# Optimization experiments

Hardware: AMD Instinct MI355X
Metric: run time of the kernel (lower is better)

The kernel has to match this reference:

```python
import jax, jax.numpy as jnp
import numpy as np

DMODEL = 1024
N_EXPERTS = 8
EXPERT_SIZE = 4096
TOPK = 2
B, S = 2, 2048


def setup_inputs() -> dict:
    key = jax.random.key(0)
    ks = jax.random.split(key, 6)
    std = EXPERT_SIZE ** (-0.5)  # init_expert_weights: normal(0, expert_size**-0.5 * weight_scale)
    x = jax.random.normal(ks[0], (B, S, DMODEL), dtype=jnp.float32)
    gate_w = 0.02 * jax.random.normal(ks[1], (N_EXPERTS, DMODEL), dtype=jnp.float32)
    w1 = std * jax.random.normal(ks[2], (N_EXPERTS, EXPERT_SIZE, DMODEL), dtype=jnp.float32)
    b1 = jnp.zeros((N_EXPERTS, EXPERT_SIZE), dtype=jnp.float32)
    w2 = std * jax.random.normal(ks[3], (N_EXPERTS, DMODEL, EXPERT_SIZE), dtype=jnp.float32)
    b2 = jnp.zeros((N_EXPERTS, DMODEL), dtype=jnp.float32)
    return {"x": x, "gate_w": gate_w, "w1": w1, "b1": b1, "w2": w2, "b2": b2}


def reference(x, gate_w, w1, b1, w2, b2):
    # Router: gate linear (no bias) -> softmax -> top-k expert selection
    logits = jnp.einsum('bsd,ed->bse', x, gate_w)          # [B,S,E]
    probs = jax.nn.softmax(logits, axis=-1)                # gate_softmax
    top_w, top_i = jax.lax.top_k(probs, TOPK)              # [B,S,K]
    # Scatter top-k weights back to a dense [B,S,E] routing matrix
    route = jnp.sum(jax.nn.one_hot(top_i, N_EXPERTS, dtype=probs.dtype)
                    * top_w[..., None], axis=-2)           # [B,S,E]
    # Per-expert 2-layer MLP (Linear -> ReLU -> Linear), combined by route weights
    out = jnp.zeros_like(x)
    for e in range(N_EXPERTS):
        h = jax.nn.relu(jnp.einsum('bsd,hd->bsh', x, w1[e]) + b1[e])  # [B,S,H]
        y = jnp.einsum('bsh,dh->bsd', h, w2[e]) + b2[e]               # [B,S,D]
        out = out + route[..., e, None] * y
    return out
```

## Files before the change

kernel.cpp:

```cpp
#include <hip/hip_runtime.h>
#include <hip/hip_bf16.h>
#include <stdint.h>

#define DMODEL 1024
#define NEXP   8
#define HSZ    4096
#define NTOK   4096
#define KSPLIT 2

typedef __attribute__((ext_vector_type(8))) short bf16x8;
typedef __attribute__((ext_vector_type(4))) float f32x4;

__device__ __forceinline__ unsigned short f2bf(float f) {
  union { float f; unsigned u; } v; v.f = f;
  return (unsigned short)((v.u + 0x8000u) >> 16);
}

__device__ __forceinline__ void gl2lds16(const void* g, void* lds) {
  __builtin_amdgcn_global_load_lds(
      (const __attribute__((address_space(1))) unsigned*)g,
      (__attribute__((address_space(3))) unsigned*)lds, 16, 0, 0);
}

__global__ __launch_bounds__(256) void cvt_all_kernel(
    const float* __restrict__ x, const float* __restrict__ w1,
    const float* __restrict__ w2, unsigned short* __restrict__ xb,
    unsigned short* __restrict__ w1b, unsigned short* __restrict__ w2b) {
  const size_t n0 = (size_t)NTOK * DMODEL / 4;
  const size_t n1 = (size_t)NEXP * HSZ * DMODEL / 4;
  size_t i = (size_t)blockIdx.x * 256 + threadIdx.x;
  const float* src; unsigned short* dst; size_t j;
  if (i < n0)            { src = x;  dst = xb;  j = i; }
  else if (i < n0 + n1)  { src = w1; dst = w1b; j = i - n0; }
  else                   { src = w2; dst = w2b; j = i - n0 - n1; }
  float4 v = ((const float4*)src)[j];
  ((ushort4*)dst)[j] = make_ushort4(f2bf(v.x), f2bf(v.y), f2bf(v.z), f2bf(v.w));
}

__global__ __launch_bounds__(256) void router_kernel(
    const float* __restrict__ x, const float* __restrict__ gw,
    int* __restrict__ cnt, int* __restrict__ tokl, float* __restrict__ twgt,
    int* __restrict__ sidx) {
  __shared__ int lcnt[NEXP];
  __shared__ int lbase[NEXP];
  __shared__ int rE[64];
  __shared__ int rS[64];
  __shared__ float rW[64];
  const int tid = threadIdx.x;
  const int wave = tid >> 6;
  const int lane = tid & 63;
  if (tid < NEXP) lcnt[tid] = 0;
  __syncthreads();

  for (int i = 0; i < 8; ++i) {
    int lt = wave * 8 + i;
    int t = blockIdx.x * 32 + lt;
    const float* xr = x + (size_t)t * DMODEL;
    float acc[NEXP];
#pragma unroll
    for (int e = 0; e < NEXP; ++e) acc[e] = 0.f;
    for (int d = lane; d < DMODEL; d += 64) {
      float xv = xr[d];
#pragma unroll
      for (int e = 0; e < NEXP; ++e) acc[e] = fmaf(xv, gw[e * DMODEL + d], acc[e]);
    }
#pragma unroll
    for (int e = 0; e < NEXP; ++e) {
#pragma unroll
      for (int o = 32; o > 0; o >>= 1) acc[e] += __shfl_down(acc[e], o);
    }
    if (lane == 0) {
      float m = acc[0];
#pragma unroll
      for (int e = 1; e < NEXP; ++e) m = fmaxf(m, acc[e]);
      float p[NEXP]; float s = 0.f;
#pragma unroll
      for (int e = 0; e < NEXP; ++e) { p[e] = __expf(acc[e] - m); s += p[e]; }
      float inv = 1.f / s;
      int i0 = 0; float b0 = p[0];
#pragma unroll
      for (int e = 1; e < NEXP; ++e) if (p[e] > b0) { b0 = p[e]; i0 = e; }
      int i1 = (i0 == 0) ? 1 : 0; float b1v = p[i1];
#pragma unroll
      for (int e = 0; e < NEXP; ++e) if (e != i0 && p[e] > b1v) { b1v = p[e]; i1 = e; }
      int s0l = atomicAdd(&lcnt[i0], 1);
      rE[lt * 2] = i0; rS[lt * 2] = s0l; rW[lt * 2] = b0 * inv;
      int s1l = atomicAdd(&lcnt[i1], 1);
      rE[lt * 2 + 1] = i1; rS[lt * 2 + 1] = s1l; rW[lt * 2 + 1] = b1v * inv;
    }
  }
  __syncthreads();
  if (tid < NEXP) lbase[tid] = atomicAdd(&cnt[tid], lcnt[tid]);
  __syncthreads();
  if (tid < 64) {
    int e = rE[tid];
    int p = lbase[e] + rS[tid];
    int t = blockIdx.x * 32 + (tid >> 1);
    tokl[e * NTOK + p] = t;
    twgt[e * NTOK + p] = rW[tid];
    sidx[2 * t + (tid & 1)] = (e << 16) | p;
  }
}

__global__ __launch_bounds__(256) void gemm1_bf_kernel(
    const unsigned short* __restrict__ Xbf, const unsigned short* __restrict__ W1bf,
    const float* __restrict__ b1, const int* __restrict__ cnt,
    const int* __restrict__ tokl, unsigned short* __restrict__ Hbuf) {
  const int e = blockIdx.z;
  const int ne = cnt[e];
  const int m0 = blockIdx.y * 128;
  if (m0 >= ne) return;
  const int n0 = blockIdx.x * 128;
  int toff = 0;
  for (int i = 0; i < NEXP; ++i) toff += (i < e) ? cnt[i] : 0;

  __shared__ __align__(16) unsigned short As[2][128 * 32];
  __shared__ __align__(16) unsigned short Bs[2][128 * 32];

  const int tid = threadIdx.x;
  const int lane = tid & 63;
  const int wave = tid >> 6;
  const int wm = (wave >> 1) * 64;
  const int wn = (wave & 1) * 64;

  const int srow = wave * 16 + (lane >> 2);
  const int scol = (((lane & 3) ^ ((lane >> 3) & 3)) << 3);
  const int* tlist = tokl + e * NTOK;
  const unsigned short* gA[2]; const unsigned short* gB[2];
  int lofs[2];
#pragma unroll
  for (int c = 0; c < 2; ++c) {
    int r = c * 64 + srow;
    int gr = m0 + r;
    int tk = tlist[(gr < ne) ? gr : 0];
    gA[c] = Xbf + (size_t)tk * DMODEL + scol;
    gB[c] = W1bf + (size_t)e * HSZ * DMODEL + (size_t)(n0 + r) * DMODEL + scol;
    lofs[c] = (c * 64 + wave * 16) * 32;
  }

  f32x4 acc[4][4];
#pragma unroll
  for (int i = 0; i < 4; ++i)
#pragma unroll
    for (int j = 0; j < 4; ++j) acc[i][j] = (f32x4){0.f, 0.f, 0.f, 0.f};

  const int fr = lane & 15;
  const int cb = lane >> 4;

#pragma unroll
  for (int c = 0; c < 2; ++c) {
    gl2lds16(gA[c], &As[0][lofs[c]]);
    gl2lds16(gB[c], &Bs[0][lofs[c]]);
  }
  __syncthreads();

  int cur = 0;
  for (int k0 = 0; k0 < DMODEL; k0 += 32) {
    const int nxt = k0 + 32;
    if (nxt < DMODEL) {
#pragma unroll
      for (int c = 0; c < 2; ++c) {
        gl2lds16(gA[c] + nxt, &As[cur ^ 1][lofs[c]]);
        gl2lds16(gB[c] + nxt, &Bs[cur ^ 1][lofs[c]]);
      }
    }
    bf16x8 af[4], bfg[4];
#pragma unroll
    for (int i = 0; i < 4; ++i) {
      int ar = wm + i * 16 + fr;
      af[i]  = *(const bf16x8*)&As[cur][ar * 32 + ((cb ^ ((ar >> 1) & 3)) << 3)];
      int br = wn + i * 16 + fr;
      bfg[i] = *(const bf16x8*)&Bs[cur][br * 32 + ((cb ^ ((br >> 1) & 3)) << 3)];
    }
#pragma unroll
    for (int i = 0; i < 4; ++i)
#pragma unroll
      for (int j = 0; j < 4; ++j)
        acc[i][j] = __builtin_amdgcn_mfma_f32_16x16x32_bf16(bfg[j], af[i], acc[i][j], 0, 0, 0);
    __syncthreads();
    cur ^= 1;
  }

  const int hq = (lane >> 4) * 4;
#pragma unroll
  for (int i = 0; i < 4; ++i) {
    int trow = m0 + wm + i * 16 + fr;
    if (trow >= ne) continue;
    size_t hrow = (size_t)(toff + trow) * HSZ;
#pragma unroll
    for (int j = 0; j < 4; ++j) {
      int hcol = n0 + wn + j * 16 + hq;
      const float* bp = b1 + e * HSZ + hcol;
      unsigned short u[4];
#pragma unroll
      for (int r = 0; r < 4; ++r)
        u[r] = f2bf(fmaxf(acc[i][j][r] + bp[r], 0.f));
      *(ushort4*)&Hbuf[hrow + hcol] = make_ushort4(u[0], u[1], u[2], u[3]);
    }
  }
}

__global__ __launch_bounds__(256) void gemm2_bf_kernel(
    const unsigned short* __restrict__ Hbuf, const unsigned short* __restrict__ W2bf,
    const int* __restrict__ cnt, const float* __restrict__ twgt,
    float* __restrict__ Ybuf) {
  const int e = blockIdx.z & 7;
  const int ks = blockIdx.z >> 3;
  const int ne = cnt[e];
  const int m0 = blockIdx.y * 128;
  if (m0 >= ne) return;
  const int n0 = blockIdx.x * 128;
  const int kbase = ks * (HSZ / KSPLIT);
  int toff = 0;
  for (int i = 0; i < NEXP; ++i) toff += (i < e) ? cnt[i] : 0;

  __shared__ __align__(16) unsigned short As[2][128 * 32];
  __shared__ __align__(16) unsigned short Bs[2][128 * 32];

  const int tid = threadIdx.x;
  const int lane = tid & 63;
  const int wave = tid >> 6;
  const int wm = (wave >> 1) * 64;
  const int wn = (wave & 1) * 64;

  const int srow = wave * 16 + (lane >> 2);
  const int scol = (((lane & 3) ^ ((lane >> 3) & 3)) << 3);
  const unsigned short* gA[2]; const unsigned short* gB[2];
  int lofs[2];
#pragma unroll
  for (int c = 0; c < 2; ++c) {
    int r = c * 64 + srow;
    int gr = m0 + r;
    int rc = (gr < ne) ? gr : 0;
    gA[c] = Hbuf + (size_t)(toff + rc) * HSZ + kbase + scol;
    gB[c] = W2bf + (size_t)e * DMODEL * HSZ + (size_t)(n0 + r) * HSZ + kbase + scol;
    lofs[c] = (c * 64 + wave * 16) * 32;
  }

  f32x4 acc[4][4];
#pragma unroll
  for (int i = 0; i < 4; ++i)
#pragma unroll
    for (int j = 0; j < 4; ++j) acc[i][j] = (f32x4){0.f, 0.f, 0.f, 0.f};

  const int fr = lane & 15;
  const int cb = lane >> 4;

#pragma unroll
  for (int c = 0; c < 2; ++c) {
    gl2lds16(gA[c], &As[0][lofs[c]]);
    gl2lds16(gB[c], &Bs[0][lofs[c]]);
  }
  __syncthreads();

  int cur = 0;
  for (int k0 = 0; k0 < HSZ / KSPLIT; k0 += 32) {
    const int nxt = k0 + 32;
    if (nxt < HSZ / KSPLIT) {
#pragma unroll
      for (int c = 0; c < 2; ++c) {
        gl2lds16(gA[c] + nxt, &As[cur ^ 1][lofs[c]]);
        gl2lds16(gB[c] + nxt, &Bs[cur ^ 1][lofs[c]]);
      }
    }
    bf16x8 af[4], bfg[4];
#pragma unroll
    for (int i = 0; i < 4; ++i) {
      int ar = wm + i * 16 + fr;
      af[i]  = *(const bf16x8*)&As[cur][ar * 32 + ((cb ^ ((ar >> 1) & 3)) << 3)];
      int br = wn + i * 16 + fr;
      bfg[i] = *(const bf16x8*)&Bs[cur][br * 32 + ((cb ^ ((br >> 1) & 3)) << 3)];
    }
#pragma unroll
    for (int i = 0; i < 4; ++i)
#pragma unroll
      for (int j = 0; j < 4; ++j)
        acc[i][j] = __builtin_amdgcn_mfma_f32_16x16x32_bf16(bfg[j], af[i], acc[i][j], 0, 0, 0);
    __syncthreads();
    cur ^= 1;
  }

  const float* wlist = twgt + e * NTOK;
  const int dq = (lane >> 4) * 4;
  float* yp = Ybuf + (size_t)ks * (2 * NTOK) * DMODEL;
#pragma unroll
  for (int i = 0; i < 4; ++i) {
    int trow = m0 + wm + i * 16 + fr;
    if (trow >= ne) continue;
    float wgt = wlist[trow];
    float* yrow = yp + (size_t)(toff + trow) * DMODEL;
#pragma unroll
    for (int j = 0; j < 4; ++j) {
      int d0 = n0 + wn + j * 16 + dq;
      float4 v = make_float4(wgt * acc[i][j][0], wgt * acc[i][j][1],
                             wgt * acc[i][j][2], wgt * acc[i][j][3]);
      *(float4*)(yrow + d0) = v;
    }
  }
}

__global__ __launch_bounds__(256) void combine_kernel(
    const float* __restrict__ Ybuf, const float* __restrict__ b2,
    const int* __restrict__ cnt, const int* __restrict__ sidx,
    const float* __restrict__ twgt, float* __restrict__ out) {
  int t = blockIdx.x;
  int offv[NEXP];
  int s = 0;
#pragma unroll
  for (int e = 0; e < NEXP; ++e) { offv[e] = s; s += cnt[e]; }
  int s0 = sidx[2 * t], s1 = sidx[2 * t + 1];
  int e0 = s0 >> 16, e1 = s1 >> 16;
  int sl0 = s0 & 0xffff, sl1 = s1 & 0xffff;
  size_t r0 = (size_t)(offv[e0] + sl0) * DMODEL;
  size_t r1 = (size_t)(offv[e1] + sl1) * DMODEL;
  float w0 = twgt[e0 * NTOK + sl0];
  float w1 = twgt[e1 * NTOK + sl1];
  const size_t PSTR = (size_t)(2 * NTOK) * DMODEL;
  int c = threadIdx.x * 4;
  float4 a0 = *(const float4*)(Ybuf + r0 + c);
  float4 a1 = *(const float4*)(Ybuf + PSTR + r0 + c);
  float4 c0 = *(const float4*)(Ybuf + r1 + c);
  float4 c1 = *(const float4*)(Ybuf + PSTR + r1 + c);
  float4 bb0 = *(const float4*)(b2 + (size_t)e0 * DMODEL + c);
  float4 bb1 = *(const float4*)(b2 + (size_t)e1 * DMODEL + c);
  *(float4*)(out + (size_t)t * DMODEL + c) = make_float4(
      a0.x + a1.x + c0.x + c1.x + w0 * bb0.x + w1 * bb1.x,
      a0.y + a1.y + c0.y + c1.y + w0 * bb0.y + w1 * bb1.y,
      a0.z + a1.z + c0.z + c1.z + w0 * bb0.z + w1 * bb1.z,
      a0.w + a1.w + c0.w + c1.w + w0 * bb0.w + w1 * bb1.w);
}

extern "C" void kernel_launch(void* const* d_in, const int* in_sizes, int n_in,
                              void* d_out, int out_size, void* d_ws, size_t ws_size,
                              hipStream_t stream) {
  const float* x  = (const float*)d_in[0];
  const float* gw = (const float*)d_in[1];
  const float* w1 = (const float*)d_in[2];
  const float* b1 = (const float*)d_in[3];
  const float* w2 = (const float*)d_in[4];
  const float* b2 = (const float*)d_in[5];
  float* out = (float*)d_out;

  char* ws = (char*)d_ws;
  int* cnt    = (int*)ws;
  int* tokl   = (int*)(ws + 128);
  float* twgt = (float*)(ws + 128 + NEXP * NTOK * 4);
  int* sidx   = (int*)(ws + 128 + 2 * NEXP * NTOK * 4);

  constexpr size_t OFF_XBF  = 327680;
  constexpr size_t OFF_W1BF = OFF_XBF  + (size_t)NTOK * DMODEL * 2;
  constexpr size_t OFF_W2BF = OFF_W1BF + (size_t)NEXP * HSZ * DMODEL * 2;
  constexpr size_t OFF_HBUF = OFF_W2BF + (size_t)NEXP * DMODEL * HSZ * 2;
  unsigned short* Xbf  = (unsigned short*)(ws + OFF_XBF);
  unsigned short* W1bf = (unsigned short*)(ws + OFF_W1BF);
  unsigned short* W2bf = (unsigned short*)(ws + OFF_W2BF);
  unsigned short* Hbuf = (unsigned short*)(ws + OFF_HBUF);
  float* Ybuf = (float*)(ws + OFF_W1BF);

  hipMemsetAsync(cnt, 0, 32, stream);
  router_kernel<<<NTOK / 32, 256, 0, stream>>>(x, gw, cnt, tokl, twgt, sidx);
  const size_t ncvt = (size_t)NTOK * DMODEL / 4 + 2 * (size_t)NEXP * HSZ * DMODEL / 4;
  cvt_all_kernel<<<(unsigned)((ncvt + 255) / 256), 256, 0, stream>>>(
      x, w1, w2, Xbf, W1bf, W2bf);
  gemm1_bf_kernel<<<dim3(HSZ / 128, NTOK / 128, NEXP), 256, 0, stream>>>(
      Xbf, W1bf, b1, cnt, tokl, Hbuf);
  gemm2_bf_kernel<<<dim3(DMODEL / 128, NTOK / 128, NEXP * KSPLIT), 256, 0, stream>>>(
      Hbuf, W2bf, cnt, twgt, Ybuf);
  combine_kernel<<<NTOK, 256, 0, stream>>>(Ybuf, b2, cnt, sidx, twgt, out);
}
```

Measured before the change: 628.8 us.

## Triple-buffer GEMM LDS pipeline and fold x bf16 conversion into router

Both expert GEMMs move from a double-buffered LDS loop with full __syncthreads to a three-stage ring. Loads are issued two steps ahead, with explicit vmcnt waits and raw s_barrier, and swizzled LDS offsets are hoisted out of the loop. This is meant to hide more global-load latency behind MFMA work, at the cost of extra LDS per block, which may lower occupancy. Separately, the router now writes the bf16 copy of x while it reads x, removing that part of the convert pass, and it processes 16 tokens per block to launch more blocks.

After: 605.9 us. 1.04x faster.

```diff
diff --git a/kernel.cpp b/kernel.cpp
--- a/kernel.cpp
+++ b/kernel.cpp
@@ -23,16 +23,13 @@
 }
 
 __global__ __launch_bounds__(256) void cvt_all_kernel(
-    const float* __restrict__ x, const float* __restrict__ w1,
-    const float* __restrict__ w2, unsigned short* __restrict__ xb,
+    const float* __restrict__ w1, const float* __restrict__ w2,
     unsigned short* __restrict__ w1b, unsigned short* __restrict__ w2b) {
-  const size_t n0 = (size_t)NTOK * DMODEL / 4;
   const size_t n1 = (size_t)NEXP * HSZ * DMODEL / 4;
   size_t i = (size_t)blockIdx.x * 256 + threadIdx.x;
   const float* src; unsigned short* dst; size_t j;
-  if (i < n0)            { src = x;  dst = xb;  j = i; }
-  else if (i < n0 + n1)  { src = w1; dst = w1b; j = i - n0; }
-  else                   { src = w2; dst = w2b; j = i - n0 - n1; }
+  if (i < n1) { src = w1; dst = w1b; j = i; }
+  else        { src = w2; dst = w2b; j = i - n1; }
   float4 v = ((const float4*)src)[j];
   ((ushort4*)dst)[j] = make_ushort4(f2bf(v.x), f2bf(v.y), f2bf(v.z), f2bf(v.w));
 }
@@ -40,27 +37,29 @@
 __global__ __launch_bounds__(256) void router_kernel(
     const float* __restrict__ x, const float* __restrict__ gw,
     int* __restrict__ cnt, int* __restrict__ tokl, float* __restrict__ twgt,
-    int* __restrict__ sidx) {
+    int* __restrict__ sidx, unsigned short* __restrict__ xb) {
   __shared__ int lcnt[NEXP];
   __shared__ int lbase[NEXP];
-  __shared__ int rE[64];
-  __shared__ int rS[64];
-  __shared__ float rW[64];
+  __shared__ int rE[32];
+  __shared__ int rS[32];
+  __shared__ float rW[32];
   const int tid = threadIdx.x;
   const int wave = tid >> 6;
   const int lane = tid & 63;
   if (tid < NEXP) lcnt[tid] = 0;
   __syncthreads();
 
-  for (int i = 0; i < 8; ++i) {
-    int lt = wave * 8 + i;
-    int t = blockIdx.x * 32 + lt;
+  for (int i = 0; i < 4; ++i) {
+    int lt = wave * 4 + i;
+    int t = blockIdx.x * 16 + lt;
     const float* xr = x + (size_t)t * DMODEL;
+    unsigned short* xbr = xb + (size_t)t * DMODEL;
     float acc[NEXP];
 #pragma unroll
     for (int e = 0; e < NEXP; ++e) acc[e] = 0.f;
     for (int d = lane; d < DMODEL; d += 64) {
       float xv = xr[d];
+      xbr[d] = f2bf(xv);
 #pragma unroll
       for (int e = 0; e < NEXP; ++e) acc[e] = fmaf(xv, gw[e * DMODEL + d], acc[e]);
     }
@@ -92,10 +91,10 @@
   __syncthreads();
   if (tid < NEXP) lbase[tid] = atomicAdd(&cnt[tid], lcnt[tid]);
   __syncthreads();
-  if (tid < 64) {
+  if (tid < 32) {
     int e = rE[tid];
     int p = lbase[e] + rS[tid];
-    int t = blockIdx.x * 32 + (tid >> 1);
+    int t = blockIdx.x * 16 + (tid >> 1);
     tokl[e * NTOK + p] = t;
     twgt[e * NTOK + p] = rW[tid];
     sidx[2 * t + (tid & 1)] = (e << 16) | p;
@@ -114,8 +113,8 @@
   int toff = 0;
   for (int i = 0; i < NEXP; ++i) toff += (i < e) ? cnt[i] : 0;
 
-  __shared__ __align__(16) unsigned short As[2][128 * 32];
-  __shared__ __align__(16) unsigned short Bs[2][128 * 32];
+  __shared__ __align__(16) unsigned short As[3][128 * 32];
+  __shared__ __align__(16) unsigned short Bs[3][128 * 32];
 
   const int tid = threadIdx.x;
   const int lane = tid & 63;
@@ -146,39 +145,58 @@
 
   const int fr = lane & 15;
   const int cb = lane >> 4;
-
+  int aoff[4], boff[4];
+#pragma unroll
+  for (int i = 0; i < 4; ++i) {
+    int ar = wm + i * 16 + fr;
+    aoff[i] = ar * 32 + ((cb ^ ((ar >> 1) & 3)) << 3);
+    int br = wn + i * 16 + fr;
+    boff[i] = br * 32 + ((cb ^ ((br >> 1) & 3)) << 3);
+  }
+
+  constexpr int NSTEP = DMODEL / 32;
 #pragma unroll
   for (int c = 0; c < 2; ++c) {
     gl2lds16(gA[c], &As[0][lofs[c]]);
     gl2lds16(gB[c], &Bs[0][lofs[c]]);
   }
-  __syncthreads();
-
-  int cur = 0;
-  for (int k0 = 0; k0 < DMODEL; k0 += 32) {
-    const int nxt = k0 + 32;
-    if (nxt < DMODEL) {
+#pragma unroll
+  for (int c = 0; c < 2; ++c) {
+    gl2lds16(gA[c] + 32, &As[1][lofs[c]]);
+    gl2lds16(gB[c] + 32, &Bs[1][lofs[c]]);
+  }
+
+  int buf = 0;
+  for (int t = 0; t < NSTEP; ++t) {
+    int nb = buf + 2; if (nb >= 3) nb -= 3;
+    if (t + 2 < NSTEP) {
+      const int s = (t + 2) * 32;
 #pragma unroll
       for (int c = 0; c < 2; ++c) {
-        gl2lds16(gA[c] + nxt, &As[cur ^ 1][lofs[c]]);
-        gl2lds16(gB[c] + nxt, &Bs[cur ^ 1][lofs[c]]);
+        gl2lds16(gA[c] + s, &As[nb][lofs[c]]);
+        gl2lds16(gB[c] + s, &Bs[nb][lofs[c]]);
       }
-    }
+      asm volatile("s_waitcnt vmcnt(8)" ::: "memory");
+    } else if (t + 1 < NSTEP) {
+      asm volatile("s_waitcnt vmcnt(4)" ::: "memory");
+    } else {
+      asm volatile("s_waitcnt vmcnt(0)" ::: "memory");
+    }
+    __builtin_amdgcn_s_barrier();
+
     bf16x8 af[4], bfg[4];
 #pragma unroll
     for (int i = 0; i < 4; ++i) {
-      int ar = wm + i * 16 + fr;
-      af[i]  = *(const bf16x8*)&As[cur][ar * 32 + ((cb ^ ((ar >> 1) & 3)) << 3)];
-      int br = wn + i * 16 + fr;
-      bfg[i] = *(const bf16x8*)&Bs[cur][br * 32 + ((cb ^ ((br >> 1) & 3)) << 3)];
+      af[i]  = *(const bf16x8*)&As[buf][aoff[i]];
+      bfg[i] = *(const bf16x8*)&Bs[buf][boff[i]];
     }
 #pragma unroll
     for (int i = 0; i < 4; ++i)
 #pragma unroll
       for (int j = 0; j < 4; ++j)
         acc[i][j] = __builtin_amdgcn_mfma_f32_16x16x32_bf16(bfg[j], af[i], acc[i][j], 0, 0, 0);
-    __syncthreads();
-    cur ^= 1;
+    __builtin_amdgcn_s_barrier();
+    buf = (buf == 2) ? 0 : buf + 1;
   }
 
   const int hq = (lane >> 4) * 4;
@@ -214,8 +232,8 @@
   int toff = 0;
   for (int i = 0; i < NEXP; ++i) toff += (i < e) ? cnt[i] : 0;
 
-  __shared__ __align__(16) unsigned short As[2][128 * 32];
-  __shared__ __align__(16) unsigned short Bs[2][128 * 32];
+  __shared__ __align__(16) unsigned short As[3][128 * 32];
+  __shared__ __align__(16) unsigned short Bs[3][128 * 32];
 
   const int tid = threadIdx.x;
   const int lane = tid & 63;
@@ -245,39 +263,58 @@
 
   const int fr = lane & 15;
   const int cb = lane >> 4;
-
+  int aoff[4], boff[4];
+#pragma unroll
+  for (int i = 0; i < 4; ++i) {
+    int ar = wm + i * 16 + fr;
+    aoff[i] = ar * 32 + ((cb ^ ((ar >> 1) & 3)) << 3);
+    int br = wn + i * 16 + fr;
+    boff[i] = br * 32 + ((cb ^ ((br >> 1) & 3)) << 3);
+  }
+
+  constexpr int NSTEP = (HSZ / KSPLIT) / 32;
 #pragma unroll
   for (int c = 0; c < 2; ++c) {
     gl2lds16(gA[c], &As[0][lofs[c]]);
     gl2lds16(gB[c], &Bs[0][lofs[c]]);
   }
-  __syncthreads();
-
-  int cur = 0;
-  for (int k0 = 0; k0 < HSZ / KSPLIT; k0 += 32) {
-    const int nxt = k0 + 32;
-    if (nxt < HSZ / KSPLIT) {
+#pragma unroll
+  for (int c = 0; c < 2; ++c) {
+    gl2lds16(gA[c] + 32, &As[1][lofs[c]]);
+    gl2lds16(gB[c] + 32, &Bs[1][lofs[c]]);
+  }
+
+  int buf = 0;
+  for (int t = 0; t < NSTEP; ++t) {
+    int nb = buf + 2; if (nb >= 3) nb -= 3;
+    if (t + 2 < NSTEP) {
+      const int s = (t + 2) * 32;
 #pragma unroll
       for (int c = 0; c < 2; ++c) {
-        gl2lds16(gA[c] + nxt, &As[cur ^ 1][lofs[c]]);
-        gl2lds16(gB[c] + nxt, &Bs[cur ^ 1][lofs[c]]);
+        gl2lds16(gA[c] + s, &As[nb][lofs[c]]);
+        gl2lds16(gB[c] + s, &Bs[nb][lofs[c]]);
       }
-    }
+      asm volatile("s_waitcnt vmcnt(8)" ::: "memory");
+    } else if (t + 1 < NSTEP) {
+      asm volatile("s_waitcnt vmcnt(4)" ::: "memory");
+    } else {
+      asm volatile("s_waitcnt vmcnt(0)" ::: "memory");
+    }
+    __builtin_amdgcn_s_barrier();
+
     bf16x8 af[4], bfg[4];
 #pragma unroll
     for (int i = 0; i < 4; ++i) {
-      int ar = wm + i * 16 + fr;
-      af[i]  = *(const bf16x8*)&As[cur][ar * 32 + ((cb ^ ((ar >> 1) & 3)) << 3)];
-      int br = wn + i * 16 + fr;
-      bfg[i] = *(const bf16x8*)&Bs[cur][br * 32 + ((cb ^ ((br >> 1) & 3)) << 3)];
+      af[i]  = *(const bf16x8*)&As[buf][aoff[i]];
+      bfg[i] = *(const bf16x8*)&Bs[buf][boff[i]];
     }
 #pragma unroll
     for (int i = 0; i < 4; ++i)
 #pragma unroll
       for (int j = 0; j < 4; ++j)
         acc[i][j] = __builtin_amdgcn_mfma_f32_16x16x32_bf16(bfg[j], af[i], acc[i][j], 0, 0, 0);
-    __syncthreads();
-    cur ^= 1;
+    __builtin_amdgcn_s_barrier();
+    buf = (buf == 2) ? 0 : buf + 1;
   }
 
   const float* wlist = twgt + e * NTOK;
@@ -358,10 +395,10 @@
   float* Ybuf = (float*)(ws + OFF_W1BF);
 
   hipMemsetAsync(cnt, 0, 32, stream);
-  router_kernel<<<NTOK / 32, 256, 0, stream>>>(x, gw, cnt, tokl, twgt, sidx);
-  const size_t ncvt = (size_t)NTOK * DMODEL / 4 + 2 * (size_t)NEXP * HSZ * DMODEL / 4;
+  router_kernel<<<NTOK / 16, 256, 0, stream>>>(x, gw, cnt, tokl, twgt, sidx, Xbf);
+  const size_t ncvt = 2 * (size_t)NEXP * HSZ * DMODEL / 4;
   cvt_all_kernel<<<(unsigned)((ncvt + 255) / 256), 256, 0, stream>>>(
-      x, w1, w2, Xbf, W1bf, W2bf);
+      w1, w2, W1bf, W2bf);
   gemm1_bf_kernel<<<dim3(HSZ / 128, NTOK / 128, NEXP), 256, 0, stream>>>(
       Xbf, W1bf, b1, cnt, tokl, Hbuf);
   gemm2_bf_kernel<<<dim3(DMODEL / 128, NTOK / 128, NEXP * KSPLIT), 256, 0, stream>>>(
```
